# Kernel optimization log

Measured on AMD Instinct MI355X. Metric: run time of the kernel, lower is better.

Reference implementation:

```python
import jax, jax.numpy as jnp
import numpy as np

B, N, C, H = 16, 4096, 384, 8
D = C // H  # head_dim = 48
WSTD = 0.02


def setup_inputs() -> dict:
    key = jax.random.key(0)
    ks = jax.random.split(key, 9)
    return {
        "x": jax.random.normal(ks[0], (B, N, C), dtype=jnp.float32),
        "conv_w": jax.random.normal(ks[1], (C, C), dtype=jnp.float32) * WSTD,  # Conv1d k=1, squeezed
        "conv_b": jax.random.normal(ks[2], (C,), dtype=jnp.float32) * WSTD,
        "wq": jax.random.normal(ks[3], (C, C), dtype=jnp.float32) * WSTD,
        "bq": jax.random.normal(ks[4], (C,), dtype=jnp.float32) * WSTD,
        "wkv": jax.random.normal(ks[5], (2 * C, C), dtype=jnp.float32) * WSTD,
        "bkv": jax.random.normal(ks[6], (2 * C,), dtype=jnp.float32) * WSTD,
        "wp": jax.random.normal(ks[7], (C, C), dtype=jnp.float32) * WSTD,
        "bp": jax.random.normal(ks[8], (C,), dtype=jnp.float32) * WSTD,
    }


def reference(x, conv_w, conv_b, wq, bq, wkv, bkv, wp, bp):
    b, n, c = x.shape
    h, d = H, c // H
    # Conv1d kernel_size=1 over channels == per-token linear: y = x @ W^T + b
    x_in = jnp.einsum("bnc,oc->bno", x, conv_w) + conv_b  # [B,N,C]
    # q: reshape(B,N,1,H,d).permute(2,0,3,4,1)[0] -> [B,H,d,N]
    q = (x_in @ wq.T + bq).reshape(b, n, h, d).transpose(0, 2, 3, 1)  # [B,H,d,N]
    kv = (x_in @ wkv.T + bkv).reshape(b, n, 2, h, d).transpose(2, 0, 3, 4, 1)  # [2,B,H,d,N]
    k, v = kv[0], kv[1]
    scale = jnp.asarray(n, x.dtype) ** -0.5  # note: N^-0.5, not head_dim^-0.5
    attn = jax.nn.softmax((q * scale) @ jnp.swapaxes(k, -2, -1), axis=-1)  # [B,H,d,d]
    out = attn @ v  # [B,H,d,N]
    # transpose(1,2) -> [B,d,H,N], then raw reshape to [B,N,C] (verbatim torch layout)
    out = jnp.transpose(out, (0, 2, 1, 3)).reshape(b, n, c)
    return out @ wp.T + bp
```

## Files before the change

kernel.cpp:

```cpp
#include <hip/hip_runtime.h>
#include <hip/hip_bf16.h>
#include <stdint.h>

#define DEVI static __device__ __forceinline__

typedef __attribute__((ext_vector_type(4))) float f32x4;
typedef __attribute__((ext_vector_type(4))) unsigned int u32x4;
typedef __attribute__((ext_vector_type(8))) short bf16x8;
typedef unsigned short u16;
typedef unsigned int u32;
typedef unsigned long long u64;

#define BB 16
#define NN 4096
#define CC 384
#define HH 8
#define DD 48

DEVI u16 f2bf(float f) {
  union { float f; u32 u; } c; c.f = f;
  u32 u = c.u;
  u32 r = (u + 0x7FFFu + ((u >> 16) & 1u)) >> 16;
  return (u16)r;
}
DEVI float bf2f(u16 h) {
  union { float f; u32 u; } c; c.u = ((u32)h) << 16;
  return c.f;
}
DEVI void stage8(u16* dst, const float* src) {
  const f32x4 a = *(const f32x4*)(src);
  const f32x4 b = *(const f32x4*)(src + 4);
  union { bf16x8 v; u16 u[8]; } o;
  o.u[0] = f2bf(a[0]); o.u[1] = f2bf(a[1]); o.u[2] = f2bf(a[2]); o.u[3] = f2bf(a[3]);
  o.u[4] = f2bf(b[0]); o.u[5] = f2bf(b[1]); o.u[6] = f2bf(b[2]); o.u[7] = f2bf(b[3]);
  *(bf16x8*)dst = o.v;
}

typedef const __attribute__((address_space(1))) void* gas_ptr;
typedef __attribute__((address_space(3))) void* las_ptr;
DEVI void gload16(const void* g, void* l) {
  __builtin_amdgcn_global_load_lds((gas_ptr)g, (las_ptr)l, 16, 0, 0);
}

__global__ __launch_bounds__(256)
void f32_to_bf16(const float* __restrict__ in, u16* __restrict__ out, int n8) {
  const int i = blockIdx.x * 256 + threadIdx.x;
  if (i >= n8) return;
  u16 tmp[8];
  stage8(tmp, in + (size_t)i * 8);
  *(bf16x8*)(out + (size_t)i * 8) = *(bf16x8*)tmp;
}

__global__ __launch_bounds__(256)
void convert_x(const float* __restrict__ x, u16* __restrict__ xb,
               u16* __restrict__ xbT) {
  __shared__ u32 LtT[64 * 68];
  const int ct = blockIdx.x, nt = blockIdx.y, b = blockIdx.z;
  const int t = threadIdx.x;
  const int n0 = nt * 128, c0 = ct * 64;
  const int coct = t & 7, c = coct * 8;
  const int q = t >> 3;

  f32x4 v[2][4];
#pragma unroll
  for (int p = 0; p < 2; ++p) {
    const int n = 2 * (p * 32 + q);
    const float* s0 = &x[((size_t)(b * NN + n0 + n)) * CC + c0 + c];
    v[p][0] = *(const f32x4*)s0;
    v[p][1] = *(const f32x4*)(s0 + 4);
    v[p][2] = *(const f32x4*)(s0 + CC);
    v[p][3] = *(const f32x4*)(s0 + CC + 4);
  }
#pragma unroll
  for (int p = 0; p < 2; ++p) {
    const int npair = p * 32 + q;
    const int n = 2 * npair;
    union { bf16x8 o; u16 e[8]; } ua, ub;
#pragma unroll
    for (int r = 0; r < 4; ++r) {
      ua.e[r] = f2bf(v[p][0][r]); ua.e[r + 4] = f2bf(v[p][1][r]);
      ub.e[r] = f2bf(v[p][2][r]); ub.e[r + 4] = f2bf(v[p][3][r]);
    }
    *(bf16x8*)&xb[((size_t)(b * NN + n0 + n)) * CC + c0 + c] = ua.o;
    *(bf16x8*)&xb[((size_t)(b * NN + n0 + n + 1)) * CC + c0 + c] = ub.o;
    const int npw = npair ^ (coct << 3);
#pragma unroll
    for (int i = 0; i < 8; ++i)
      LtT[(c + i) * 68 + npw] = (u32)ua.e[i] | ((u32)ub.e[i] << 16);
  }
  __syncthreads();
#pragma unroll
  for (int p = 0; p < 4; ++p) {
    const int id = p * 256 + t;
    const int cc2 = id >> 4, ng = id & 15;
    const int co2 = (cc2 >> 3) & 7;
    union { u32x4 q4; bf16x8 o; } u;
    u.q4 = *(const u32x4*)&LtT[cc2 * 68 + ((ng * 4) ^ (co2 << 3))];
    *(bf16x8*)&xbT[((size_t)(b * CC + c0 + cc2)) * NN + n0 + ng * 8] = u.o;
  }
}

__global__ __launch_bounds__(256)
void transpose_cw(const float* __restrict__ cw, u16* __restrict__ cwT) {
  __shared__ u32 LtT[64 * 33];
  const int mt = blockIdx.x, ct = blockIdx.y;
  const int t = threadIdx.x;
  const int m0 = mt * 64, c0 = ct * 64;
  const int cl = (t & 15) * 4;
  const int mp = t >> 4;
#pragma unroll
  for (int pass = 0; pass < 2; ++pass) {
    const int w = mp + pass * 16;
    const int m = w * 2;
    const float* s0 = &cw[(size_t)(m0 + m) * CC + c0 + cl];
    const f32x4 a = *(const f32x4*)s0;
    const f32x4 bv = *(const f32x4*)(s0 + CC);
#pragma unroll
    for (int i = 0; i < 4; ++i)
      LtT[(cl + i) * 33 + w] = (u32)f2bf(a[i]) | ((u32)f2bf(bv[i]) << 16);
  }
  __syncthreads();
#pragma unroll
  for (int pass = 0; pass < 2; ++pass) {
    const int v = pass * 256 + t;
    const int c = v >> 3, mg = v & 7;
    union { bf16x8 o; u32 q[4]; } u;
#pragma unroll
    for (int r = 0; r < 4; ++r) u.q[r] = LtT[c * 33 + mg * 4 + r];
    *(bf16x8*)&cwT[(size_t)(c0 + c) * CC + m0 + mg * 8] = u.o;
  }
}

__global__ __launch_bounds__(256)
void bias_fuse(const float* __restrict__ wq, const float* __restrict__ bq,
               const float* __restrict__ wkv, const float* __restrict__ bkv,
               const float* __restrict__ cb, float* __restrict__ bf_) {
  const int o = blockIdx.x * 4 + (threadIdx.x >> 6);
  const int lane = threadIdx.x & 63;
  const float* wrow;
  float b0;
  if (o < CC) { wrow = wq + (size_t)o * CC;        b0 = bq[o]; }
  else        { wrow = wkv + (size_t)(o - CC) * CC; b0 = bkv[o - CC]; }
  float s = 0.f;
  for (int m = lane; m < CC; m += 64) s += wrow[m] * cb[m];
#pragma unroll
  for (int off = 32; off; off >>= 1) s += __shfl_xor(s, off, 64);
  if (lane == 0) bf_[o] = b0 + s;
}

__global__ __launch_bounds__(256)
void colsum(const u16* __restrict__ xbT, float* __restrict__ sx) {
  const int b = blockIdx.y, c = blockIdx.x * 16 + (threadIdx.x >> 4);
  const int sl = threadIdx.x & 15;
  const u16* src = xbT + ((size_t)(b * CC + c)) * NN + sl * 256;
  float s = 0.f;
  for (int i = 0; i < 32; ++i) {
    const bf16x8 v = *(const bf16x8*)(src + i * 8);
#pragma unroll
    for (int r = 0; r < 8; ++r) s += bf2f((u16)v[r]);
  }
#pragma unroll
  for (int m = 1; m < 16; m <<= 1) s += __shfl_xor(s, m, 64);
  if (sl == 0) sx[b * CC + c] = s;
}

__global__ __launch_bounds__(128)
void proj_sx(const u16* __restrict__ Wf, const float* __restrict__ sx,
             float* __restrict__ P) {
  __shared__ float sl[CC];
  const int b = blockIdx.y, o = blockIdx.x * 128 + threadIdx.x;
  for (int i = threadIdx.x; i < CC; i += 128) sl[i] = sx[b * CC + i];
  __syncthreads();
  float acc = 0.f;
  const u16* wr = Wf + (size_t)o * CC;
  for (int c8 = 0; c8 < CC; c8 += 8) {
    const bf16x8 w = *(const bf16x8*)(wr + c8);
#pragma unroll
    for (int r = 0; r < 8; ++r) acc += bf2f((u16)w[r]) * sl[c8 + r];
  }
  P[b * 768 + o] = acc;
}

template<typename OT, int BIASMODE, int TRI = 0, int SWZ = 1>
__global__ __launch_bounds__(512)
void gemm_f(const u16* __restrict__ A, const u16* __restrict__ W,
            const float* __restrict__ bias, OT* __restrict__ C,
            int M, int N, int K, int klen, int nbn, int nbm, int tpb,
            long sA, long sW, long sC, long sCp, long sBias) {
  constexpr int BK = 64;
  __shared__ __align__(16) u16 smem[32768];

  const int nx = gridDim.x;
  const int lin = blockIdx.x;
  const int lin2 = SWZ ? (lin & 7) * (nx >> 3) + (lin >> 3) : lin;
  const int b = lin2 / tpb;
  int t2 = lin2 % tpb;
  int bn, bm, p;
  if constexpr (TRI) {
    const int tl = t2 % 6; p = t2 / 6;
    bm = tl < 3 ? 0 : (tl < 5 ? 1 : 2);
    bn = tl < 3 ? tl : (tl < 5 ? tl - 2 : 2);
  } else {
    bn = t2 % nbn; t2 /= nbn;
    bm = t2 % nbm;
    p = t2 / nbm;
  }
  A += (size_t)b * sA; W += (size_t)b * sW;
  C += (size_t)b * sC + (size_t)p * sCp;
  if (BIASMODE) bias += (size_t)b * sBias;

  const int t = threadIdx.x;
  const int wid = t >> 6, lane = t & 63;
  const int wr = wid >> 2, wc = wid & 3;
  const int row0 = bm * 128, col0 = bn * 128;
  const int lrow = lane & 15;
  const int lswz = (lane & 7) << 3;
  const int kstart = p * klen;

  const int arow = t >> 3;
  const int scol = ((t & 7) ^ ((t >> 3) & 7)) * 8;
  const u16* Ag = A + (size_t)(row0 + arow) * K + scol;
  const u16* Wg = W + (size_t)(col0 + arow) * K + scol;

  f32x4 acc[4][2] = {};
  const int NT = klen >> 6;

  auto stage = [&](int buf, int kt) {
    u16* Al = smem + buf * 16384 + t * 8;
    u16* Bl = smem + buf * 16384 + 8192 + t * 8;
    const int k0 = kstart + kt * BK;
#pragma unroll
    for (int it = 0; it < 2; ++it) {
      gload16(Ag + (size_t)(it * 64) * K + k0, Al + it * 4096);
      gload16(Wg + (size_t)(it * 64) * K + k0, Bl + it * 4096);
    }
  };

  stage(0, 0);
  __syncthreads();
  int cur = 0;
  for (int kt = 0; kt < NT; ++kt) {
    if (kt + 1 < NT) stage(cur ^ 1, kt + 1);
    const u16* As = smem + cur * 16384;
    const u16* Bs = smem + cur * 16384 + 8192;
#pragma unroll
    for (int kk = 0; kk < 2; ++kk) {
      const int lk = (kk * 32 + (lane >> 4) * 8) ^ lswz;
      bf16x8 af[4], bfv[2];
#pragma unroll
      for (int i = 0; i < 4; ++i)
        af[i] = *(const bf16x8*)&As[(wr * 64 + i * 16 + lrow) * BK + lk];
#pragma unroll
      for (int j = 0; j < 2; ++j)
        bfv[j] = *(const bf16x8*)&Bs[(wc * 32 + j * 16 + lrow) * BK + lk];
#pragma unroll
      for (int i = 0; i < 4; ++i)
#pragma unroll
        for (int j = 0; j < 2; ++j)
          acc[i][j] = __builtin_amdgcn_mfma_f32_16x16x32_bf16(af[i], bfv[j], acc[i][j], 0, 0, 0);
    }
    __syncthreads();
    cur ^= 1;
  }

  const int lr = (lane >> 4) * 4;
  if constexpr (sizeof(OT) == 2) {
    u16* Ct = smem;
#pragma unroll
    for (int i = 0; i < 4; ++i)
#pragma unroll
      for (int j = 0; j < 2; ++j) {
        const int ccol = wc * 32 + j * 16 + lrow;
        float bv = 0.f;
        if constexpr (BIASMODE == 1) bv = bias[col0 + ccol];
#pragma unroll
        for (int r = 0; r < 4; ++r) {
          const int rrow = wr * 64 + i * 16 + lr + r;
          float b2 = bv;
          if constexpr (BIASMODE == 2) b2 = bias[row0 + rrow];
          Ct[rrow * 132 + ccol] = f2bf(acc[i][j][r] + b2);
        }
      }
    __syncthreads();
#pragma unroll
    for (int it = 0; it < 4; ++it) {
      const int id = it * 512 + t;
      const int row = id >> 4, c16 = (id & 15) * 8;
      *(bf16x8*)((u16*)C + (size_t)(row0 + row) * N + col0 + c16) =
          *(const bf16x8*)&Ct[row * 132 + c16];
    }
  } else {
    const int orow = row0 + wr * 64, ocol = col0 + wc * 32;
#pragma unroll
    for (int i = 0; i < 4; ++i)
#pragma unroll
      for (int j = 0; j < 2; ++j) {
        const int cc2 = ocol + j * 16 + lrow;
        float bv = 0.f;
        if constexpr (BIASMODE == 1) bv = bias[cc2];
#pragma unroll
        for (int r = 0; r < 4; ++r) {
          const int rr = orow + i * 16 + lr + r;
          float b2 = bv;
          if constexpr (BIASMODE == 2) b2 = bias[rr];
          C[(size_t)rr * N + cc2] = acc[i][j][r] + b2;
        }
      }
  }
}

__global__ __launch_bounds__(256)
void reduceG(const float* __restrict__ Gp, u16* __restrict__ Gbf) {
  const int b = blockIdx.y;
  const int e = blockIdx.x * 256 + threadIdx.x;
  const int i = e / CC, j = e % CC;
  const int ee = (i <= j) ? e : (j * CC + i);
  const float* s = Gp + (size_t)b * 4 * 147456 + ee;
  Gbf[(size_t)b * 147456 + e] =
      f2bf(s[0] + s[147456] + s[2 * 147456] + s[3 * 147456]);
}

__global__ __launch_bounds__(256)
void s_softmax(const u16* __restrict__ M1g, const u16* __restrict__ Wf,
               const float* __restrict__ bf_, const float* __restrict__ P,
               const u16* __restrict__ UvT, u16* __restrict__ AUb,
               float* __restrict__ rbias) {
  __shared__ float Sf[48 * 52];
  __shared__ __align__(16) u16 att[48 * 56];
  const int bh = blockIdx.x, b = bh >> 3, h = bh & 7;
  const int t = threadIdx.x, wid = t >> 6, lane = t & 63;
  const int lrow = lane & 15, lkq = lane >> 4;

  if (wid < 3) {
    f32x4 acc[3] = {};
    const u16* Arow = M1g + (size_t)b * 147456 + (size_t)(h * 48 + wid * 16 + lrow) * CC;
    const u16* Brow = Wf + (size_t)(CC + h * 48) * CC;
    for (int ks = 0; ks < 12; ++ks) {
      const int k = ks * 32 + lkq * 8;
      const bf16x8 af = *(const bf16x8*)(Arow + k);
#pragma unroll
      for (int j = 0; j < 3; ++j) {
        const bf16x8 bfr = *(const bf16x8*)(Brow + (size_t)(j * 16 + lrow) * CC + k);
        acc[j] = __builtin_amdgcn_mfma_f32_16x16x32_bf16(af, bfr, acc[j], 0, 0, 0);
      }
    }
    const int lr = lkq * 4;
#pragma unroll
    for (int j = 0; j < 3; ++j)
#pragma unroll
      for (int r = 0; r < 4; ++r)
        Sf[(wid * 16 + lr + r) * 52 + j * 16 + lrow] = acc[j][r];
  }
  __syncthreads();

  if (t < 48) {
    const float bi = bf_[h * 48 + t];
    const float pq = P[b * 768 + h * 48 + t];
    float row[48];
    float mx = -1e30f;
#pragma unroll
    for (int j = 0; j < 48; ++j) {
      const float g = bf_[CC + h * 48 + j];
      const float pk = P[b * 768 + CC + h * 48 + j];
      const float s = (Sf[t * 52 + j] + bi * pk + pq * g + 4096.f * bi * g) * 0.015625f;
      row[j] = s;
      mx = fmaxf(mx, s);
    }
    float sum = 0.f;
#pragma unroll
    for (int j = 0; j < 48; ++j) { row[j] = __expf(row[j] - mx); sum += row[j]; }
    const float inv = 1.f / sum;
    float rb = 0.f;
#pragma unroll
    for (int j = 0; j < 48; ++j) {
      const float a = row[j] * inv;
      att[t * 56 + j] = f2bf(a);
      rb += a * bf_[2 * CC + h * 48 + j];
    }
#pragma unroll
    for (int j = 48; j < 56; ++j) att[t * 56 + j] = 0;
    rbias[b * CC + t * 8 + h] = rb;
  }
  __syncthreads();

  f32x4 acc[3][6] = {};
  const u16* Vbase = UvT + h * 48;
  const bf16x8 z = {};
#pragma unroll
  for (int kk = 0; kk < 2; ++kk) {
    const int k = kk * 32 + lkq * 8;
    bf16x8 af[3];
#pragma unroll
    for (int i = 0; i < 3; ++i) {
      af[i] = *(const bf16x8*)&att[(i * 16 + lrow) * 56 + k];
      if (k >= 48) af[i] = z;
    }
#pragma unroll
    for (int ct = 0; ct < 6; ++ct) {
      const int c = wid * 96 + ct * 16 + lrow;
      bf16x8 bfr = *(const bf16x8*)(Vbase + (size_t)c * CC + k);
      if (k >= 48) bfr = z;
#pragma unroll
      for (int i = 0; i < 3; ++i)
        acc[i][ct] = __builtin_amdgcn_mfma_f32_16x16x32_bf16(af[i], bfr, acc[i][ct], 0, 0, 0);
    }
  }
  const int lr = lkq * 4;
#pragma unroll
  for (int i = 0; i < 3; ++i)
#pragma unroll
    for (int ct = 0; ct < 6; ++ct) {
      const int c = wid * 96 + ct * 16 + lrow;
#pragma unroll
      for (int r = 0; r < 4; ++r) {
        const int ii = i * 16 + lr + r;
        AUb[(size_t)b * 147456 + (size_t)(ii * 8 + h) * CC + c] = f2bf(acc[i][ct][r]);
      }
    }
}

extern "C" void kernel_launch(void* const* d_in, const int* in_sizes, int n_in,
                              void* d_out, int out_size, void* d_ws, size_t ws_size,
                              hipStream_t stream) {
  const float* x      = (const float*)d_in[0];
  const float* conv_w = (const float*)d_in[1];
  const float* conv_b = (const float*)d_in[2];
  const float* wq     = (const float*)d_in[3];
  const float* bq     = (const float*)d_in[4];
  const float* wkv    = (const float*)d_in[5];
  const float* bkv    = (const float*)d_in[6];
  const float* wp     = (const float*)d_in[7];
  const float* bp     = (const float*)d_in[8];
  float* y = (float*)d_out;

  char* ws = (char*)d_ws;
  u16*   Wf    = (u16*)(ws + 0);
  float* bf_   = (float*)(ws + 884736);
  u16*   wpb   = (u16*)(ws + 889344);
  u16*   UvT   = (u16*)(ws + 1184256);
  float* sx    = (float*)(ws + 1479168);
  float* P     = (float*)(ws + 1503744);
  float* rb    = (float*)(ws + 1552896);
  u16*   M1g   = (u16*)(ws + 1577472);
  u16*   Gbf   = (u16*)(ws + 6296064);
  u16*   AUb   = (u16*)(ws + 11014656);
  float* Gpart = (float*)(ws + 15733248);
  u16*   wtopb = (u16*)(ws + 53481984);
  u16*   cwTb  = (u16*)(ws + 54366720);
  u16*   xb    = (u16*)(ws + 54661632);
  u16*   xbT   = (u16*)(ws + 104993280);
  u16*   R     = xbT;

  convert_x<<<dim3(6, 32, 16), dim3(256), 0, stream>>>(x, xb, xbT);
  f32_to_bf16<<<dim3(72), dim3(256), 0, stream>>>(wp, wpb, (CC * CC) / 8);
  f32_to_bf16<<<dim3(72), dim3(256), 0, stream>>>(wq, wtopb, (CC * CC) / 8);
  f32_to_bf16<<<dim3(144), dim3(256), 0, stream>>>(wkv, wtopb + CC * CC,
                                                   (2 * CC * CC) / 8);
  transpose_cw<<<dim3(6, 6), dim3(256), 0, stream>>>(conv_w, cwTb);
  bias_fuse<<<dim3(288), dim3(256), 0, stream>>>(wq, bq, wkv, bkv, conv_b, bf_);
  gemm_f<u16, 0, 0, 0><<<dim3(18), dim3(512), 0, stream>>>(
      wtopb, cwTb, nullptr, Wf, 2 * CC, CC, CC, CC, 3, 6, 18,
      0, 0, 0, 0, 0);
  gemm_f<u16, 0, 0, 0><<<dim3(9), dim3(512), 0, stream>>>(
      cwTb, wtopb + 2 * CC * CC, nullptr, UvT, CC, CC, CC, CC, 3, 3, 9,
      0, 0, 0, 0, 0);
  colsum<<<dim3(24, 16), dim3(256), 0, stream>>>(xbT, sx);
  proj_sx<<<dim3(6, 16), dim3(128), 0, stream>>>(Wf, sx, P);
  gemm_f<float, 0, 1><<<dim3(384), dim3(512), 0, stream>>>(
      xbT, xbT, nullptr, Gpart, CC, CC, NN, 1024, 3, 3, 24,
      (long)CC * NN, (long)CC * NN, 4L * 147456, 147456, 0);
  reduceG<<<dim3(576, 16), dim3(256), 0, stream>>>(Gpart, Gbf);
  gemm_f<u16, 0><<<dim3(144), dim3(512), 0, stream>>>(
      Wf, Gbf, nullptr, M1g, CC, CC, CC, CC, 3, 3, 9,
      0, 147456, 147456, 0, 0);
  s_softmax<<<dim3(128), dim3(256), 0, stream>>>(M1g, Wf, bf_, P, UvT, AUb, rb);
  gemm_f<u16, 2><<<dim3(1536), dim3(512), 0, stream>>>(
      AUb, xb, rb, R, CC, NN, CC, CC, 32, 3, 96,
      147456, (long)NN * CC, (long)NN * CC, 0, CC);
  gemm_f<float, 1><<<dim3(1536), dim3(512), 0, stream>>>(
      R, wpb, bp, y, BB * NN, CC, CC, CC, 3, 512, 1536,
      0, 0, 0, 0, 0);
}
```

Baseline: 223.2 us.

## Drop transposed x copy; compute Gram and column sums from row-major bf16 x

Removes the convert_x kernel that wrote both a row-major and a transposed bf16 copy of x, and replaces it with a plain f32-to-bf16 conversion. A new gram_x kernel computes the X^T X partial Gram matrices directly from row-major x. It transposes tiles through registers into swizzled LDS and reuses the A tile for diagonal blocks. colsum is rewritten to reduce over rows of the row-major layout. This saves a full write and read of the transposed x buffer (about 50 MB), at the cost of a hand-written Gram kernel with in-LDS transposition that may use MFMA less efficiently than the generic GEMM.

After: 229.6 us. 1.03x slower.

```diff
diff --git a/kernel.cpp b/kernel.cpp
--- a/kernel.cpp
+++ b/kernel.cpp
@@ -49,55 +49,6 @@
   u16 tmp[8];
   stage8(tmp, in + (size_t)i * 8);
   *(bf16x8*)(out + (size_t)i * 8) = *(bf16x8*)tmp;
-}
-
-__global__ __launch_bounds__(256)
-void convert_x(const float* __restrict__ x, u16* __restrict__ xb,
-               u16* __restrict__ xbT) {
-  __shared__ u32 LtT[64 * 68];
-  const int ct = blockIdx.x, nt = blockIdx.y, b = blockIdx.z;
-  const int t = threadIdx.x;
-  const int n0 = nt * 128, c0 = ct * 64;
-  const int coct = t & 7, c = coct * 8;
-  const int q = t >> 3;
-
-  f32x4 v[2][4];
-#pragma unroll
-  for (int p = 0; p < 2; ++p) {
-    const int n = 2 * (p * 32 + q);
-    const float* s0 = &x[((size_t)(b * NN + n0 + n)) * CC + c0 + c];
-    v[p][0] = *(const f32x4*)s0;
-    v[p][1] = *(const f32x4*)(s0 + 4);
-    v[p][2] = *(const f32x4*)(s0 + CC);
-    v[p][3] = *(const f32x4*)(s0 + CC + 4);
-  }
-#pragma unroll
-  for (int p = 0; p < 2; ++p) {
-    const int npair = p * 32 + q;
-    const int n = 2 * npair;
-    union { bf16x8 o; u16 e[8]; } ua, ub;
-#pragma unroll
-    for (int r = 0; r < 4; ++r) {
-      ua.e[r] = f2bf(v[p][0][r]); ua.e[r + 4] = f2bf(v[p][1][r]);
-      ub.e[r] = f2bf(v[p][2][r]); ub.e[r + 4] = f2bf(v[p][3][r]);
-    }
-    *(bf16x8*)&xb[((size_t)(b * NN + n0 + n)) * CC + c0 + c] = ua.o;
-    *(bf16x8*)&xb[((size_t)(b * NN + n0 + n + 1)) * CC + c0 + c] = ub.o;
-    const int npw = npair ^ (coct << 3);
-#pragma unroll
-    for (int i = 0; i < 8; ++i)
-      LtT[(c + i) * 68 + npw] = (u32)ua.e[i] | ((u32)ub.e[i] << 16);
-  }
-  __syncthreads();
-#pragma unroll
-  for (int p = 0; p < 4; ++p) {
-    const int id = p * 256 + t;
-    const int cc2 = id >> 4, ng = id & 15;
-    const int co2 = (cc2 >> 3) & 7;
-    union { u32x4 q4; bf16x8 o; } u;
-    u.q4 = *(const u32x4*)&LtT[cc2 * 68 + ((ng * 4) ^ (co2 << 3))];
-    *(bf16x8*)&xbT[((size_t)(b * CC + c0 + cc2)) * NN + n0 + ng * 8] = u.o;
-  }
 }
 
 __global__ __launch_bounds__(256)
@@ -149,19 +100,28 @@
 }
 
 __global__ __launch_bounds__(256)
-void colsum(const u16* __restrict__ xbT, float* __restrict__ sx) {
-  const int b = blockIdx.y, c = blockIdx.x * 16 + (threadIdx.x >> 4);
-  const int sl = threadIdx.x & 15;
-  const u16* src = xbT + ((size_t)(b * CC + c)) * NN + sl * 256;
-  float s = 0.f;
-  for (int i = 0; i < 32; ++i) {
-    const bf16x8 v = *(const bf16x8*)(src + i * 8);
-#pragma unroll
-    for (int r = 0; r < 8; ++r) s += bf2f((u16)v[r]);
-  }
-#pragma unroll
-  for (int m = 1; m < 16; m <<= 1) s += __shfl_xor(s, m, 64);
-  if (sl == 0) sx[b * CC + c] = s;
+void colsum(const u16* __restrict__ xb, float* __restrict__ sx) {
+  __shared__ float red[256][8];
+  const int b = blockIdx.y, c0 = blockIdx.x * 64;
+  const int t = threadIdx.x;
+  const int c8 = t & 7, ns = t >> 3;
+  const u16* src = xb + (size_t)b * NN * CC + c0 + c8 * 8;
+  float a[8] = {};
+  for (int it = 0; it < 128; ++it) {
+    const bf16x8 v = *(const bf16x8*)(src + (size_t)(ns + 32 * it) * CC);
+#pragma unroll
+    for (int r = 0; r < 8; ++r) a[r] += bf2f((u16)v[r]);
+  }
+#pragma unroll
+  for (int r = 0; r < 8; ++r) red[t][r] = a[r];
+  __syncthreads();
+  if (t < 64) {
+    const int c8o = t >> 3, e = t & 7;
+    float s = 0.f;
+#pragma unroll
+    for (int n2 = 0; n2 < 32; ++n2) s += red[c8o + 8 * n2][e];
+    sx[b * CC + c0 + c8o * 8 + e] = s;
+  }
 }
 
 __global__ __launch_bounds__(128)
@@ -179,6 +139,108 @@
     for (int r = 0; r < 8; ++r) acc += bf2f((u16)w[r]) * sl[c8 + r];
   }
   P[b * 768 + o] = acc;
+}
+
+__global__ __launch_bounds__(256)
+void gram_x(const u16* __restrict__ xb, float* __restrict__ Gpart) {
+  __shared__ u32 lds[2 * 128 * 36];
+  const int nx = gridDim.x;
+  const int lin = blockIdx.x;
+  const int lin2 = (lin & 7) * (nx >> 3) + (lin >> 3);
+  const int b = lin2 / 24;
+  const int t2 = lin2 % 24;
+  const int tl = t2 % 6, p = t2 / 6;
+  const int bm = tl < 3 ? 0 : (tl < 5 ? 1 : 2);
+  const int bn = tl < 3 ? tl : (tl < 5 ? tl - 2 : 2);
+  const bool diag = (bm == bn);
+  const u16* X = xb + (size_t)b * NN * CC;
+  float* C = Gpart + (size_t)b * 4 * 147456 + (size_t)p * 147456;
+
+  const int t = threadIdx.x;
+  const int wid = t >> 6, lane = t & 63;
+  const int wr = wid >> 1, wc = wid & 1;
+  const int lrow = lane & 15;
+  const int coct = t & 15;
+  const int npb = t >> 4;
+  u32* As = lds;
+  u32* Bs = lds + 128 * 36;
+  const u32* Bsr = diag ? As : Bs;
+
+  f32x4 acc[4][4] = {};
+  const int n00 = p * 1024;
+
+  bf16x8 rA[2][2], rB[2][2];
+  auto loadregs = [&](int kt) {
+    const int n0 = n00 + kt * 64;
+#pragma unroll
+    for (int k = 0; k < 2; ++k) {
+      const int n = n0 + 2 * (npb + 16 * k);
+      const u16* sa = X + (size_t)n * CC + bm * 128 + coct * 8;
+      rA[k][0] = *(const bf16x8*)sa;
+      rA[k][1] = *(const bf16x8*)(sa + CC);
+      if (!diag) {
+        const u16* sb = X + (size_t)n * CC + bn * 128 + coct * 8;
+        rB[k][0] = *(const bf16x8*)sb;
+        rB[k][1] = *(const bf16x8*)(sb + CC);
+      }
+    }
+  };
+  auto writeregs = [&]() {
+    const int swz = (coct & 7) << 2;
+#pragma unroll
+    for (int k = 0; k < 2; ++k) {
+      const int npw = (npb + 16 * k) ^ swz;
+      union { bf16x8 v; u16 e[8]; } a0, a1, b0, b1;
+      a0.v = rA[k][0]; a1.v = rA[k][1];
+      b0.v = rB[k][0]; b1.v = rB[k][1];
+#pragma unroll
+      for (int i = 0; i < 8; ++i) {
+        const int addr = (coct * 8 + i) * 36 + npw;
+        As[addr] = (u32)(u16)a0.e[i] | ((u32)(u16)a1.e[i] << 16);
+        if (!diag) Bs[addr] = (u32)(u16)b0.e[i] | ((u32)(u16)b1.e[i] << 16);
+      }
+    }
+  };
+
+  loadregs(0);
+  for (int kt = 0; kt < 16; ++kt) {
+    writeregs();
+    __syncthreads();
+    if (kt + 1 < 16) loadregs(kt + 1);
+#pragma unroll
+    for (int kk = 0; kk < 2; ++kk) {
+      const int w0 = kk * 16 + (lane >> 4) * 4;
+      bf16x8 af[4], bfv[4];
+#pragma unroll
+      for (int i = 0; i < 4; ++i) {
+        const int r = wr * 64 + i * 16 + lrow;
+        af[i] = *(const bf16x8*)&As[r * 36 + (w0 ^ (((r >> 3) & 7) << 2))];
+      }
+#pragma unroll
+      for (int j = 0; j < 4; ++j) {
+        const int r = wc * 64 + j * 16 + lrow;
+        bfv[j] = *(const bf16x8*)&Bsr[r * 36 + (w0 ^ (((r >> 3) & 7) << 2))];
+      }
+#pragma unroll
+      for (int i = 0; i < 4; ++i)
+#pragma unroll
+        for (int j = 0; j < 4; ++j)
+          acc[i][j] = __builtin_amdgcn_mfma_f32_16x16x32_bf16(af[i], bfv[j], acc[i][j], 0, 0, 0);
+    }
+    __syncthreads();
+  }
+
+  const int lr = (lane >> 4) * 4;
+  const int orow = bm * 128 + wr * 64, ocol = bn * 128 + wc * 64;
+#pragma unroll
+  for (int i = 0; i < 4; ++i)
+#pragma unroll
+    for (int j = 0; j < 4; ++j) {
+      const int cc2 = ocol + j * 16 + lrow;
+#pragma unroll
+      for (int r = 0; r < 4; ++r)
+        C[(size_t)(orow + i * 16 + lr + r) * CC + cc2] = acc[i][j][r];
+    }
 }
 
 template<typename OT, int BIASMODE, int TRI = 0, int SWZ = 1>
@@ -448,10 +510,10 @@
   u16*   wtopb = (u16*)(ws + 53481984);
   u16*   cwTb  = (u16*)(ws + 54366720);
   u16*   xb    = (u16*)(ws + 54661632);
-  u16*   xbT   = (u16*)(ws + 104993280);
-  u16*   R     = xbT;
-
-  convert_x<<<dim3(6, 32, 16), dim3(256), 0, stream>>>(x, xb, xbT);
+  u16*   R     = (u16*)(ws + 104993280);
+
+  f32_to_bf16<<<dim3((BB * NN * CC) / 8 / 256), dim3(256), 0, stream>>>(
+      x, xb, (BB * NN * CC) / 8);
   f32_to_bf16<<<dim3(72), dim3(256), 0, stream>>>(wp, wpb, (CC * CC) / 8);
   f32_to_bf16<<<dim3(72), dim3(256), 0, stream>>>(wq, wtopb, (CC * CC) / 8);
   f32_to_bf16<<<dim3(144), dim3(256), 0, stream>>>(wkv, wtopb + CC * CC,
@@ -464,11 +526,9 @@
   gemm_f<u16, 0, 0, 0><<<dim3(9), dim3(512), 0, stream>>>(
       cwTb, wtopb + 2 * CC * CC, nullptr, UvT, CC, CC, CC, CC, 3, 3, 9,
       0, 0, 0, 0, 0);
-  colsum<<<dim3(24, 16), dim3(256), 0, stream>>>(xbT, sx);
+  colsum<<<dim3(6, 16), dim3(256), 0, stream>>>(xb, sx);
   proj_sx<<<dim3(6, 16), dim3(128), 0, stream>>>(Wf, sx, P);
-  gemm_f<float, 0, 1><<<dim3(384), dim3(512), 0, stream>>>(
-      xbT, xbT, nullptr, Gpart, CC, CC, NN, 1024, 3, 3, 24,
-      (long)CC * NN, (long)CC * NN, 4L * 147456, 147456, 0);
+  gram_x<<<dim3(384), dim3(256), 0, stream>>>(xb, Gpart);
   reduceG<<<dim3(576, 16), dim3(256), 0, stream>>>(Gpart, Gbf);
   gemm_f<u16, 0><<<dim3(144), dim3(512), 0, stream>>>(
       Wf, Gbf, nullptr, M1g, CC, CC, CC, CC, 3, 3, 9,
```
